# Kernel tuning notes

Measured on AMD Instinct MI355X. Metric: run time of the kernel, lower is better.

Reference implementation:

```python
import jax, jax.numpy as jnp
import numpy as np

WS = [2048, 4096, 8192]
RS = [1, 2, 4]
OFFSET = 0
NEG = -1e30


def _causal_attn(xseg, Wq, Wk, Wv, Wo):
    """xseg: (b, s, m, c). Returns (out (b,s,m,c), denom (b,s,m)) where denom is
    the softmax denominator sum_j exp(score_ij) per query (computed stably via lse)."""
    c = xseg.shape[-1]
    m = xseg.shape[-2]
    q = jnp.einsum('bsmc,cd->bsmd', xseg, Wq)
    k = jnp.einsum('bsmc,cd->bsmd', xseg, Wk)
    v = jnp.einsum('bsmc,cd->bsmd', xseg, Wv)
    scores = jnp.einsum('bsid,bsjd->bsij', q, k) / jnp.sqrt(jnp.asarray(c, xseg.dtype))
    causal = jnp.tril(jnp.ones((m, m), dtype=bool))
    scores = jnp.where(causal, scores, NEG)
    lse = jax.nn.logsumexp(scores, axis=-1)            # (b,s,m)
    p = jnp.exp(scores - lse[..., None])               # softmax
    o = jnp.einsum('bsij,bsjd->bsid', p, v)
    o = jnp.einsum('bsid,dc->bsic', o, Wo)
    return o, jnp.exp(lse)


def setup_inputs() -> dict:
    key = jax.random.key(0)
    kx, kq, kk, kv, ko = jax.random.split(key, 5)
    b, n, c = 4, 8192, 128
    scale = 1.0 / np.sqrt(c)  # keep activations O(1) so exp(lse) stays finite
    return {
        'x': jax.random.normal(kx, (b, n, c), dtype=jnp.float32),
        'Wq': jax.random.normal(kq, (c, c), dtype=jnp.float32) * scale,
        'Wk': jax.random.normal(kk, (c, c), dtype=jnp.float32) * scale,
        'Wv': jax.random.normal(kv, (c, c), dtype=jnp.float32) * scale,
        'Wo': jax.random.normal(ko, (c, c), dtype=jnp.float32) * scale,
    }


def reference(x, Wq, Wk, Wv, Wo):
    b, n, c = x.shape
    denom_sums = jnp.zeros((b, n), dtype=x.dtype)
    branches = []
    for w, r in zip(WS, RS):
        s = n // w
        # gather dilated tokens within each segment: (b, s, m, c)
        xr = x.reshape(b, s, w, c)[:, :, OFFSET::r, :]
        m = xr.shape[2]
        o, d = _causal_attn(xr, Wq, Wk, Wv, Wo)
        # global positions of the gathered tokens, flattened over (segment, within-seg)
        idx = (jnp.arange(s)[:, None] * w + OFFSET + r * jnp.arange(m)[None, :]).reshape(-1)
        d_flat = d.reshape(b, s * m)
        o_flat = o.reshape(b, s * m, c)
        denom_sums = denom_sums.at[:, idx].add(d_flat)
        branches.append((idx, o_flat, d_flat))
    out = jnp.zeros_like(x)
    for idx, o_flat, d_flat in branches:
        alpha = d_flat / denom_sums[:, idx]             # (b, s*m)
        out = out.at[:, idx].add(o_flat * alpha[..., None])
    return out
```

## Files before the change

kernel.cpp:

```cpp
#include <hip/hip_runtime.h>
#include <hip/hip_bf16.h>

typedef __attribute__((ext_vector_type(8))) __bf16 bf16x8;
typedef __attribute__((ext_vector_type(4))) float f32x4;
typedef __attribute__((ext_vector_type(8))) unsigned short u16x8;

#define DEVI __device__ __forceinline__
#define MFMA(a,b,c) __builtin_amdgcn_mfma_f32_16x16x32_bf16((a),(b),(c),0,0,0)
#define EXP2F(x) __builtin_exp2f(x)
#define LOG2F(x) __builtin_log2f(x)

DEVI unsigned short f2bf(float f){ __bf16 h = (__bf16)f; return __builtin_bit_cast(unsigned short, h); }
DEVI float bf2f(unsigned short u){ unsigned int x = ((unsigned int)u) << 16; return __builtin_bit_cast(float, x); }
DEVI bf16x8 ld_bf8(const void* p){ u16x8 u = *(const u16x8*)p; return __builtin_bit_cast(bf16x8, u); }
DEVI f32x4 splat4(float x){ f32x4 v = {x,x,x,x}; return v; }
DEVI f32x4 vmax4(f32x4 a, f32x4 b){
  f32x4 r;
  #pragma unroll
  for (int i=0;i<4;++i) r[i]=fmaxf(a[i],b[i]);
  return r;
}
DEVI void gload_lds16(const void* g, void* l){
  void* g2 = const_cast<void*>(g);
  __builtin_amdgcn_global_load_lds((__attribute__((address_space(1))) void*)g2,
                                   (__attribute__((address_space(3))) void*)l, 16, 0, 0);
}
#if __has_builtin(__builtin_amdgcn_permlane16_swap) && __has_builtin(__builtin_amdgcn_permlane32_swap)
DEVI float wavemax_hi(float x){
  unsigned int xu = __builtin_bit_cast(unsigned int, x);
  auto r1 = __builtin_amdgcn_permlane16_swap(xu, xu, false, false);
  float m = fmaxf(__builtin_bit_cast(float, (unsigned int)r1[0]),
                  __builtin_bit_cast(float, (unsigned int)r1[1]));
  unsigned int mu = __builtin_bit_cast(unsigned int, m);
  auto r2 = __builtin_amdgcn_permlane32_swap(mu, mu, false, false);
  return fmaxf(__builtin_bit_cast(float, (unsigned int)r2[0]),
               __builtin_bit_cast(float, (unsigned int)r2[1]));
}
#else
DEVI float wavemax_hi(float x){
  x = fmaxf(x, __shfl_xor(x, 16, 64));
  x = fmaxf(x, __shfl_xor(x, 32, 64));
  return x;
}
#endif

__device__ const unsigned int SCHED[30] = {
  0x100C000Bu, 0x110C0C0Bu, 0x050C0005u, 0x1C0B0A0Fu, 0x1D0B150Fu,
  0x0E0B000Au, 0x0F0B0B0Au, 0x1B0A000Fu, 0x180A000Eu, 0x190A0A0Eu,
  0x1A0A140Eu, 0x170A120Du, 0x0C0A0009u, 0x0D0A0A09u, 0x040A0004u,
  0x1509000Du, 0x1609090Du, 0x1309080Cu, 0x1409110Cu, 0x0A090008u,
  0x0B090908u, 0x1208000Cu, 0x08080007u, 0x09080807u, 0x03080003u,
  0x06070006u, 0x07070706u, 0x02060002u, 0x01040001u, 0x00020000u
};
__device__ const int CB[16] = {0,1,2,3,4,5,6,8,10,12,14,16,18,21,24,27};

__global__ __launch_bounds__(256) void k_prep(const float* __restrict__ Wq, const float* __restrict__ Wk,
                                              const float* __restrict__ Wv, const float* __restrict__ Wo,
                                              unsigned short* __restrict__ wT){
  int i = blockIdx.x*256 + threadIdx.x;
  int mat = i >> 14, col = (i >> 7) & 127, k = i & 127;
  const float* W = (mat==0)?Wq:(mat==1)?Wk:(mat==2)?Wv:Wo;
  float v = W[k*128 + col];
  if (mat == 0) v *= 0.12754245006257017f;
  wT[i] = f2bf(v);
}

__global__ __launch_bounds__(512) void k_qkv(const float* __restrict__ x, const unsigned short* __restrict__ wT,
                                             unsigned short* __restrict__ Qo, unsigned short* __restrict__ Ko,
                                             unsigned short* __restrict__ VT0, unsigned short* __restrict__ VT1,
                                             unsigned short* __restrict__ VT2){
  __shared__ unsigned short Tl[128*130];
  const int tid=threadIdx.x, lane=tid&63, wid=tid>>6, ll=lane&15, hi=lane>>4;
  const int row0g = blockIdx.x*128;
  const long row0 = (long)row0g + wid*16;
  bf16x8 a[4];
  {
    const float* xr = x + (row0 + ll)*128 + hi*8;
    #pragma unroll
    for (int ks=0;ks<4;++ks){
      f32x4 f0 = *(const f32x4*)(const void*)(xr + ks*32);
      f32x4 f1 = *(const f32x4*)(const void*)(xr + ks*32 + 4);
      u16x8 u;
      #pragma unroll
      for (int j=0;j<4;++j){ u[j]=f2bf(f0[j]); u[j+4]=f2bf(f1[j]); }
      a[ks] = __builtin_bit_cast(bf16x8, u);
    }
  }
  #pragma unroll
  for (int m3=0;m3<3;++m3){
    const unsigned short* wp = wT + m3*16384 + ll*128 + hi*8;
    #pragma unroll
    for (int nt=0;nt<8;++nt){
      f32x4 acc=splat4(0.f);
      #pragma unroll
      for (int ks=0;ks<4;++ks){
        bf16x8 b = ld_bf8(wp + nt*2048 + ks*32);
        acc = MFMA(a[ks], b, acc);
      }
      if (m3 < 2){
        unsigned short* outp = (m3==0)?Qo:Ko;
        #pragma unroll
        for (int r=0;r<4;++r)
          outp[(row0 + hi*4 + r)*128 + nt*16 + ll] = f2bf(acc[r]);
      } else {
        #pragma unroll
        for (int r=0;r<4;++r)
          Tl[(wid*16 + hi*4 + r)*130 + nt*16 + ll] = f2bf(acc[r]);
      }
    }
  }
  __syncthreads();
  int tk = 2*lane;
  int pp0 = (tk>>5)*32 + ((tk>>4)&1)*4 + ((tk&15)>>2)*8 + (tk&3);
  #pragma unroll 4
  for (int p=0;p<16;++p){
    int d = wid*16 + p;
    unsigned int w0 = (unsigned int)Tl[(2*lane)*130 + d] | ((unsigned int)Tl[(2*lane+1)*130 + d] << 16);
    *(unsigned int*)(VT0 + (long)d*32768 + row0g + pp0) = w0;
    if (lane < 32){
      unsigned int w1 = (unsigned int)Tl[(4*lane)*130 + d] | ((unsigned int)Tl[(4*lane+2)*130 + d] << 16);
      *(unsigned int*)(VT1 + (long)d*16384 + (row0g>>1) + pp0) = w1;
    }
    if (lane < 16){
      unsigned int w2 = (unsigned int)Tl[(8*lane)*130 + d] | ((unsigned int)Tl[(8*lane+4)*130 + d] << 16);
      *(unsigned int*)(VT2 + (long)d*8192 + (row0g>>2) + pp0) = w2;
    }
  }
}

__global__ __launch_bounds__(256,3) void k_attn(
    const unsigned short* __restrict__ Qg, const unsigned short* __restrict__ Kg,
    const unsigned short* __restrict__ VT0, const unsigned short* __restrict__ VT1,
    const unsigned short* __restrict__ VT2,
    unsigned short* __restrict__ OP, float* __restrict__ LP){
  __shared__ unsigned char smem[49152];

  const int tid=threadIdx.x, lane=tid&63, wid=tid>>6, ll=lane&15, hi=lane>>4;

  int x = blockIdx.x & 7;
  int i = blockIdx.x >> 3;
  int sid, r;
  if (i < 60){
    r = i >> 2; int k = i & 3;
    if (k < 3){ sid = 3*x + k; }
    else { sid = 24 + (x >> 1); if (x & 1) r += 15; }
  } else {
    int t = i - 60; r = 15 + t/3; sid = 3*x + t%3;
  }
  unsigned int e = SCHED[r];
  int qb   = (int)(e & 255u);
  int t032 = (int)((e >> 8) & 255u) * 2;
  int n32  = (int)((e >> 16) & 255u) * 2;
  int slot = (int)(e >> 24);
  int br, bb, seg;
  if (sid < 16){ br=0; bb=sid>>2; seg=sid&3; }
  else if (sid < 24){ br=1; bb=(sid-16)>>1; seg=(sid-16)&1; }
  else { br=2; bb=sid-24; seg=0; }
  const int rstr = 1 << br;
  const long g0 = (long)bb*8192 + (long)seg*(2048 << br);
  const int P = sid*30 + slot;
  const unsigned short* VTb = (br==0)?VT0:(br==1)?VT1:VT2;
  const int NC = 32768 >> br;
  const int rb0 = (int)(g0 >> br);

  const int qrow_w = qb*128 + wid*32;

  bf16x8 aq[2][4];
  #pragma unroll
  for (int mt=0;mt<2;++mt){
    long gq = g0 + (long)rstr*(qrow_w + mt*16 + ll);
    const unsigned short* qp = Qg + gq*128 + hi*8;
    #pragma unroll
    for (int ks=0;ks<4;++ks) aq[mt][ks] = ld_bf8(qp + ks*32);
  }

  f32x4 o[2][8];
  #pragma unroll
  for (int mt=0;mt<2;++mt){
    #pragma unroll
    for (int dt=0;dt<8;++dt) o[mt][dt]=splat4(0.f);
  }
  float mrun[2], lrun[2];
  mrun[0]=mrun[1]=0.f; lrun[0]=lrun[1]=0.f;

  const int m7 = ll & 7;
  int koffs[4];
  #pragma unroll
  for (int ks=0;ks<4;++ks) koffs[ks] = ll*256 + (((ks*4 + hi) ^ m7) * 16);
  const int voffb = ll*64 + (((hi + (ll >> 1)) & 3) * 16);

  const long kadv = (long)rstr*32*128;
  const unsigned short* ksrc0 = Kg + (g0 + (long)rstr*((long)t032*32 + wid*8 + hi))*128 + ((ll ^ hi) * 8);
  const unsigned short* ksrc1 = Kg + (g0 + (long)rstr*((long)t032*32 + wid*8 + 4 + hi))*128 + ((ll ^ (4 + hi)) * 8);
  const int d0_ = tid >> 2,        s0_ = tid & 3,        ga_ = (s0_ - (d0_ >> 1)) & 3;
  const int d1_ = (256+tid) >> 2,  s1_ = tid & 3,        gb_ = (s1_ - (d1_ >> 1)) & 3;
  const unsigned short* vsrc0 = VTb + (long)d0_*NC + rb0 + t032*32 + ga_*8;
  const unsigned short* vsrc1 = VTb + (long)d1_*NC + rb0 + t032*32 + gb_*8;

#define STAGE(bslot)                                                                   \
  {                                                                                    \
    unsigned char* Kb = smem + (bslot)*8192;                                           \
    unsigned char* Vb = smem + 24576 + (bslot)*8192;                                   \
    gload_lds16((const void*)ksrc0, (void*)(Kb + wid*2048));                           \
    gload_lds16((const void*)ksrc1, (void*)(Kb + wid*2048 + 1024));                    \
    gload_lds16((const void*)vsrc0, (void*)(Vb + wid*1024));                           \
    gload_lds16((const void*)vsrc1, (void*)(Vb + 4096 + wid*1024));                    \
    ksrc0 += kadv; ksrc1 += kadv; vsrc0 += 32; vsrc1 += 32;                            \
  }

  STAGE(0);
  STAGE(1);

  for (int it=0; it<n32; ++it){
    const int kt = t032 + it;
    if (it + 1 < n32){
      asm volatile("s_waitcnt vmcnt(4) lgkmcnt(0)" ::: "memory");
    } else {
      asm volatile("s_waitcnt vmcnt(0) lgkmcnt(0)" ::: "memory");
    }
    __builtin_amdgcn_s_barrier();
    __builtin_amdgcn_sched_barrier(0);

    if (it + 2 < n32){
      STAGE((it + 2) % 3);
    }

    if (kt*32 <= qrow_w + 31){
      unsigned char* Kc = smem + (it % 3)*8192;
      unsigned char* Vc = smem + 24576 + (it % 3)*8192;
      f32x4 s[2][2];
      #pragma unroll
      for (int mt=0;mt<2;++mt){
        #pragma unroll
        for (int nt=0;nt<2;++nt) s[mt][nt]=splat4(0.f);
      }
      #pragma unroll
      for (int nt=0;nt<2;++nt){
        #pragma unroll
        for (int ks=0;ks<4;++ks){
          bf16x8 bk = ld_bf8(Kc + koffs[ks] + nt*4096);
          s[0][nt] = MFMA(bk, aq[0][ks], s[0][nt]);
          s[1][nt] = MFMA(bk, aq[1][ks], s[1][nt]);
        }
      }
      if (kt*32 + 31 > qrow_w){
        #pragma unroll
        for (int mt=0;mt<2;++mt){
          int qrow = qrow_w + mt*16 + ll;
          #pragma unroll
          for (int nt=0;nt<2;++nt){
            int kvcol = kt*32 + nt*16 + hi*4;
            #pragma unroll
            for (int rr=0;rr<4;++rr) if (kvcol + rr > qrow) s[mt][nt][rr] = -1e30f;
          }
        }
      }
      bf16x8 pa[2];
      #pragma unroll
      for (int mt=0;mt<2;++mt){
        f32x4 ps[2];
        #pragma unroll
        for (int nt=0;nt<2;++nt){
          #pragma unroll
          for (int rr=0;rr<4;++rr) ps[nt][rr] = EXP2F(s[mt][nt][rr] - mrun[mt]);
        }
        f32x4 t4 = vmax4(s[mt][0], s[mt][1]);
        float mloc = fmaxf(fmaxf(t4[0],t4[1]), fmaxf(t4[2],t4[3]));
        mloc = wavemax_hi(mloc);
        bool upd = __any(mloc > mrun[mt] + 8.0f);
        float mnew = upd ? fmaxf(mrun[mt], mloc) : mrun[mt];
        float psc  = upd ? EXP2F(mrun[mt] - mnew) : 1.0f;
        mrun[mt] = mnew;
        f32x4 tsum = ps[0] + ps[1];
        lrun[mt] = psc * (lrun[mt] + (tsum[0]+tsum[1]) + (tsum[2]+tsum[3]));
        if (upd){
          f32x4 scv;
          #pragma unroll
          for (int rr=0;rr<4;++rr) scv[rr] = __shfl(psc, hi*4 + rr, 64);
          #pragma unroll
          for (int dt=0;dt<8;++dt) o[mt][dt] = o[mt][dt]*scv;
        }
        u16x8 up;
        #pragma unroll
        for (int rr=0;rr<4;++rr){
          up[rr]   = f2bf(ps[0][rr] * psc);
          up[4+rr] = f2bf(ps[1][rr] * psc);
        }
        pa[mt] = __builtin_bit_cast(bf16x8, up);
      }
      #pragma unroll
      for (int dt=0;dt<8;++dt){
        bf16x8 bv = ld_bf8(Vc + voffb + dt*1024);
        o[0][dt] = MFMA(pa[0], bv, o[0][dt]);
        o[1][dt] = MFMA(pa[1], bv, o[1][dt]);
      }
    }
  }
#undef STAGE

  unsigned short* op = OP + (long)P*16384;
  float* lp = LP + (long)P*128;
  #pragma unroll
  for (int mt=0;mt<2;++mt){
    float l = lrun[mt];
    l += __shfl_xor(l, 16, 64);
    l += __shfl_xor(l, 32, 64);
    float invs = 1.f / l;
    f32x4 iv;
    #pragma unroll
    for (int rr=0;rr<4;++rr) iv[rr] = __shfl(invs, hi*4 + rr, 64);
    #pragma unroll
    for (int dt=0;dt<8;++dt){
      f32x4 res = o[mt][dt]*iv;
      #pragma unroll
      for (int rr=0;rr<4;++rr){
        int qloc = wid*32 + mt*16 + hi*4 + rr;
        op[qloc*128 + dt*16 + ll] = f2bf(res[rr]);
      }
    }
    float lse = mrun[mt] + LOG2F(l);
    if (lane < 16){
      lp[wid*32 + mt*16 + lane] = lse;
    }
  }
}

__global__ __launch_bounds__(256) void k_comb(
    const unsigned short* __restrict__ OP, const float* __restrict__ LP,
    const unsigned short* __restrict__ wT, float* __restrict__ out){
  __shared__ float Wl[9*32];
  __shared__ unsigned short Tl[32*136];
  const int tid = threadIdx.x;
  const long G0 = (long)blockIdx.x * 32;
  const int bb = (int)(G0 >> 13);
  const int P0 = (int)(G0 & 8191);

  int pb[3], bn[3], qlb[3];
  {
    int sid0 = bb*4 + (P0 >> 11); int qb0 = (P0 & 2047) >> 7;
    pb[0] = sid0*30 + CB[qb0]; bn[0] = (qb0<6)?1:(qb0<12)?2:3; qlb[0] = P0 & 127;
    int p1b = P0 >> 1; int sid1 = 16 + bb*2 + (p1b >> 11); int qb1 = (p1b & 2047) >> 7;
    pb[1] = sid1*30 + CB[qb1]; bn[1] = (qb1<6)?1:(qb1<12)?2:3; qlb[1] = p1b & 127;
    int p2b = P0 >> 2; int sid2 = 24 + bb; int qb2 = p2b >> 7;
    pb[2] = sid2*30 + CB[qb2]; bn[2] = (qb2<6)?1:(qb2<12)?2:3; qlb[2] = p2b & 127;
  }

  if (tid < 32){
    int i = tid;
    float Lx[9];
    #pragma unroll
    for (int b=0;b<3;++b){
      bool pv = (i & ((1<<b)-1)) == 0;
      int ql = qlb[b] + (i >> b);
      #pragma unroll
      for (int c=0;c<3;++c){
        bool v = pv && (c < bn[b]);
        Lx[b*3+c] = v ? LP[(pb[b]+c)*128 + ql] : -1e30f;
      }
    }
    float mx = -1e30f;
    #pragma unroll
    for (int s=0;s<9;++s) mx = fmaxf(mx, Lx[s]);
    float W[9]; float wsum = 0.f;
    #pragma unroll
    for (int b=0;b<3;++b){
      bool pv = (i & ((1<<b)-1)) == 0;
      #pragma unroll
      for (int c=0;c<3;++c){
        bool v = pv && (c < bn[b]);
        W[b*3+c] = v ? EXP2F(Lx[b*3+c] - mx) : 0.f;
        wsum += W[b*3+c];
      }
    }
    float inv = 1.f / wsum;
    #pragma unroll
    for (int s=0;s<9;++s) Wl[s*32 + i] = W[s] * inv;
  }
  __syncthreads();

  {
    const int ch = tid & 15;
    const int r0 = tid >> 4;
    #pragma unroll
    for (int p=0;p<2;++p){
      int row = p*16 + r0;
      float y[8];
      #pragma unroll
      for (int j=0;j<8;++j) y[j] = 0.f;
      #pragma unroll
      for (int b=0;b<3;++b){
        if ((row & ((1<<b)-1)) == 0){
          int opr = qlb[b] + (row >> b);
          for (int c=0;c<bn[b];++c){
            float wgt = Wl[(b*3+c)*32 + row];
            const unsigned short* pp = OP + (long)(pb[b]+c)*16384 + opr*128 + ch*8;
            u16x8 u = *(const u16x8*)(const void*)pp;
            #pragma unroll
            for (int j=0;j<8;++j) y[j] += wgt * bf2f(u[j]);
          }
        }
      }
      u16x8 o;
      #pragma unroll
      for (int j=0;j<8;++j) o[j] = f2bf(y[j]);
      *(u16x8*)(void*)(Tl + row*136 + ch*8) = o;
    }
  }
  __syncthreads();

  {
    const int wv = tid >> 6, lane = tid & 63, ll = lane & 15, hi = lane >> 4;
    bf16x8 a[2][4];
    #pragma unroll
    for (int mt=0;mt<2;++mt){
      #pragma unroll
      for (int ks=0;ks<4;++ks)
        a[mt][ks] = ld_bf8(Tl + (mt*16 + ll)*136 + ks*32 + hi*8);
    }
    const unsigned short* wp = wT + 3*16384 + ll*128 + hi*8;
    #pragma unroll
    for (int t=0;t<2;++t){
      int nt = wv*2 + t;
      f32x4 acc0=splat4(0.f), acc1=splat4(0.f);
      #pragma unroll
      for (int ks=0;ks<4;++ks){
        bf16x8 b = ld_bf8(wp + nt*2048 + ks*32);
        acc0 = MFMA(a[0][ks], b, acc0);
        acc1 = MFMA(a[1][ks], b, acc1);
      }
      #pragma unroll
      for (int rr=0;rr<4;++rr){
        out[(G0 + hi*4 + rr)*128 + nt*16 + ll]      = acc0[rr];
        out[(G0 + 16 + hi*4 + rr)*128 + nt*16 + ll] = acc1[rr];
      }
    }
  }
}

extern "C" void kernel_launch(void* const* d_in, const int* in_sizes, int n_in,
                              void* d_out, int out_size, void* d_ws, size_t ws_size,
                              hipStream_t stream){
  const float* x  = (const float*)d_in[0];
  const float* Wq = (const float*)d_in[1];
  const float* Wk = (const float*)d_in[2];
  const float* Wv = (const float*)d_in[3];
  const float* Wo = (const float*)d_in[4];
  char* ws = (char*)d_ws;
  unsigned short* wT  = (unsigned short*)(ws);
  unsigned short* Q   = (unsigned short*)(ws + 131072);
  unsigned short* K   = (unsigned short*)(ws + 8519680);
  unsigned short* VT0 = (unsigned short*)(ws + 16908288);
  unsigned short* VT1 = (unsigned short*)(ws + 25296896);
  unsigned short* VT2 = (unsigned short*)(ws + 29491200);
  unsigned short* OP  = (unsigned short*)(ws + 31588352);
  float* LP           = (float*)(ws + 59113472);
  k_prep<<<256, 256, 0, stream>>>(Wq, Wk, Wv, Wo, wT);
  k_qkv <<<256, 512, 0, stream>>>(x, wT, Q, K, VT0, VT1, VT2);
  k_attn<<<840, 256, 0, stream>>>(Q, K, VT0, VT1, VT2, OP, LP);
  k_comb<<<1024, 256, 0, stream>>>(OP, LP, wT, (float*)d_out);
}
```

Before: 107.9 us.

## Split attention block across 8 waves of 16 query rows each

The attention kernel now uses 512 threads per block, with each wave owning 16 query rows instead of 32. The K/V staging per thread is halved to one K and one V load, and the wait count is adjusted to match. The online softmax now rescales before the exponent and starts the running max at -1e30. This gives more waves for latency hiding and fewer registers per wave, at the cost of each K/V LDS fragment being reused across fewer MFMAs per wave and more waves reading the same LDS data.

New measurement: 106.0 us. About the same (-1.8%).

```diff
diff --git a/kernel.cpp b/kernel.cpp
--- a/kernel.cpp
+++ b/kernel.cpp
@@ -128,7 +128,7 @@
   }
 }
 
-__global__ __launch_bounds__(256,3) void k_attn(
+__global__ __launch_bounds__(512,4) void k_attn(
     const unsigned short* __restrict__ Qg, const unsigned short* __restrict__ Kg,
     const unsigned short* __restrict__ VT0, const unsigned short* __restrict__ VT1,
     const unsigned short* __restrict__ VT2,
@@ -163,25 +163,20 @@
   const int NC = 32768 >> br;
   const int rb0 = (int)(g0 >> br);
 
-  const int qrow_w = qb*128 + wid*32;
-
-  bf16x8 aq[2][4];
+  const int qrow_w = qb*128 + wid*16;
+
+  bf16x8 aq[4];
+  {
+    long gq = g0 + (long)rstr*(qrow_w + ll);
+    const unsigned short* qp = Qg + gq*128 + hi*8;
+    #pragma unroll
+    for (int ks=0;ks<4;++ks) aq[ks] = ld_bf8(qp + ks*32);
+  }
+
+  f32x4 o[8];
   #pragma unroll
-  for (int mt=0;mt<2;++mt){
-    long gq = g0 + (long)rstr*(qrow_w + mt*16 + ll);
-    const unsigned short* qp = Qg + gq*128 + hi*8;
-    #pragma unroll
-    for (int ks=0;ks<4;++ks) aq[mt][ks] = ld_bf8(qp + ks*32);
-  }
-
-  f32x4 o[2][8];
-  #pragma unroll
-  for (int mt=0;mt<2;++mt){
-    #pragma unroll
-    for (int dt=0;dt<8;++dt) o[mt][dt]=splat4(0.f);
-  }
-  float mrun[2], lrun[2];
-  mrun[0]=mrun[1]=0.f; lrun[0]=lrun[1]=0.f;
+  for (int dt=0;dt<8;++dt) o[dt]=splat4(0.f);
+  float mrun=-1e30f, lrun=0.f;
 
   const int m7 = ll & 7;
   int koffs[4];
@@ -190,22 +185,18 @@
   const int voffb = ll*64 + (((hi + (ll >> 1)) & 3) * 16);
 
   const long kadv = (long)rstr*32*128;
-  const unsigned short* ksrc0 = Kg + (g0 + (long)rstr*((long)t032*32 + wid*8 + hi))*128 + ((ll ^ hi) * 8);
-  const unsigned short* ksrc1 = Kg + (g0 + (long)rstr*((long)t032*32 + wid*8 + 4 + hi))*128 + ((ll ^ (4 + hi)) * 8);
-  const int d0_ = tid >> 2,        s0_ = tid & 3,        ga_ = (s0_ - (d0_ >> 1)) & 3;
-  const int d1_ = (256+tid) >> 2,  s1_ = tid & 3,        gb_ = (s1_ - (d1_ >> 1)) & 3;
-  const unsigned short* vsrc0 = VTb + (long)d0_*NC + rb0 + t032*32 + ga_*8;
-  const unsigned short* vsrc1 = VTb + (long)d1_*NC + rb0 + t032*32 + gb_*8;
+  const int krow_s = wid*4 + hi;
+  const unsigned short* ksrc = Kg + (g0 + (long)rstr*((long)t032*32 + krow_s))*128 + ((ll ^ (krow_s & 7)) * 8);
+  const int d0_ = tid >> 2, s0_ = tid & 3, ga_ = (s0_ - (d0_ >> 1)) & 3;
+  const unsigned short* vsrc = VTb + (long)d0_*NC + rb0 + t032*32 + ga_*8;
 
 #define STAGE(bslot)                                                                   \
   {                                                                                    \
     unsigned char* Kb = smem + (bslot)*8192;                                           \
     unsigned char* Vb = smem + 24576 + (bslot)*8192;                                   \
-    gload_lds16((const void*)ksrc0, (void*)(Kb + wid*2048));                           \
-    gload_lds16((const void*)ksrc1, (void*)(Kb + wid*2048 + 1024));                    \
-    gload_lds16((const void*)vsrc0, (void*)(Vb + wid*1024));                           \
-    gload_lds16((const void*)vsrc1, (void*)(Vb + 4096 + wid*1024));                    \
-    ksrc0 += kadv; ksrc1 += kadv; vsrc0 += 32; vsrc1 += 32;                            \
+    gload_lds16((const void*)ksrc, (void*)(Kb + wid*1024));                            \
+    gload_lds16((const void*)vsrc, (void*)(Vb + wid*1024));                            \
+    ksrc += kadv; vsrc += 32;                                                          \
   }
 
   STAGE(0);
@@ -214,7 +205,7 @@
   for (int it=0; it<n32; ++it){
     const int kt = t032 + it;
     if (it + 1 < n32){
-      asm volatile("s_waitcnt vmcnt(4) lgkmcnt(0)" ::: "memory");
+      asm volatile("s_waitcnt vmcnt(2) lgkmcnt(0)" ::: "memory");
     } else {
       asm volatile("s_waitcnt vmcnt(0) lgkmcnt(0)" ::: "memory");
     }
@@ -225,74 +216,67 @@
       STAGE((it + 2) % 3);
     }
 
-    if (kt*32 <= qrow_w + 31){
+    if (kt*32 <= qrow_w + 15){
       unsigned char* Kc = smem + (it % 3)*8192;
       unsigned char* Vc = smem + 24576 + (it % 3)*8192;
-      f32x4 s[2][2];
-      #pragma unroll
-      for (int mt=0;mt<2;++mt){
-        #pragma unroll
-        for (int nt=0;nt<2;++nt) s[mt][nt]=splat4(0.f);
-      }
+      f32x4 s[2];
+      s[0]=splat4(0.f); s[1]=splat4(0.f);
       #pragma unroll
       for (int nt=0;nt<2;++nt){
         #pragma unroll
         for (int ks=0;ks<4;++ks){
           bf16x8 bk = ld_bf8(Kc + koffs[ks] + nt*4096);
-          s[0][nt] = MFMA(bk, aq[0][ks], s[0][nt]);
-          s[1][nt] = MFMA(bk, aq[1][ks], s[1][nt]);
+          s[nt] = MFMA(bk, aq[ks], s[nt]);
         }
       }
       if (kt*32 + 31 > qrow_w){
-        #pragma unroll
-        for (int mt=0;mt<2;++mt){
-          int qrow = qrow_w + mt*16 + ll;
+        int qrow = qrow_w + ll;
+        #pragma unroll
+        for (int nt=0;nt<2;++nt){
+          int kvcol = kt*32 + nt*16 + hi*4;
           #pragma unroll
-          for (int nt=0;nt<2;++nt){
-            int kvcol = kt*32 + nt*16 + hi*4;
-            #pragma unroll
-            for (int rr=0;rr<4;++rr) if (kvcol + rr > qrow) s[mt][nt][rr] = -1e30f;
-          }
-        }
-      }
-      bf16x8 pa[2];
-      #pragma unroll
-      for (int mt=0;mt<2;++mt){
-        f32x4 ps[2];
+          for (int rr=0;rr<4;++rr) if (kvcol + rr > qrow) s[nt][rr] = -1e30f;
+        }
+      }
+      {
+        f32x4 t4 = vmax4(s[0], s[1]);
+        float mloc = fmaxf(fmaxf(t4[0],t4[1]), fmaxf(t4[2],t4[3]));
+        mloc = wavemax_hi(mloc);
+        bool upd = __any(mloc > mrun + 8.0f);
+        if (upd){
+          float mnew = fmaxf(mrun, mloc);
+          float sc = EXP2F(mrun - mnew);
+          mrun = mnew;
+          lrun *= sc;
+          f32x4 scv;
+          #pragma unroll
+          for (int rr=0;rr<4;++rr) scv[rr] = __shfl(sc, hi*4 + rr, 64);
+          #pragma unroll
+          for (int dt=0;dt<8;++dt) o[dt] = o[dt]*scv;
+        }
+        f32x4 tsum = splat4(0.f);
         #pragma unroll
         for (int nt=0;nt<2;++nt){
           #pragma unroll
-          for (int rr=0;rr<4;++rr) ps[nt][rr] = EXP2F(s[mt][nt][rr] - mrun[mt]);
-        }
-        f32x4 t4 = vmax4(s[mt][0], s[mt][1]);
-        float mloc = fmaxf(fmaxf(t4[0],t4[1]), fmaxf(t4[2],t4[3]));
-        mloc = wavemax_hi(mloc);
-        bool upd = __any(mloc > mrun[mt] + 8.0f);
-        float mnew = upd ? fmaxf(mrun[mt], mloc) : mrun[mt];
-        float psc  = upd ? EXP2F(mrun[mt] - mnew) : 1.0f;
-        mrun[mt] = mnew;
-        f32x4 tsum = ps[0] + ps[1];
-        lrun[mt] = psc * (lrun[mt] + (tsum[0]+tsum[1]) + (tsum[2]+tsum[3]));
-        if (upd){
-          f32x4 scv;
-          #pragma unroll
-          for (int rr=0;rr<4;++rr) scv[rr] = __shfl(psc, hi*4 + rr, 64);
-          #pragma unroll
-          for (int dt=0;dt<8;++dt) o[mt][dt] = o[mt][dt]*scv;
-        }
+          for (int rr=0;rr<4;++rr) s[nt][rr] = EXP2F(s[nt][rr] - mrun);
+          tsum += s[nt];
+        }
+        lrun += (tsum[0]+tsum[1]) + (tsum[2]+tsum[3]);
+      }
+      bf16x8 pa;
+      {
         u16x8 up;
         #pragma unroll
         for (int rr=0;rr<4;++rr){
-          up[rr]   = f2bf(ps[0][rr] * psc);
-          up[4+rr] = f2bf(ps[1][rr] * psc);
-        }
-        pa[mt] = __builtin_bit_cast(bf16x8, up);
+          up[rr]   = f2bf(s[0][rr]);
+          up[4+rr] = f2bf(s[1][rr]);
+        }
+        pa = __builtin_bit_cast(bf16x8, up);
       }
       #pragma unroll
       for (int dt=0;dt<8;++dt){
         bf16x8 bv = ld_bf8(Vc + voffb + dt*1024);
-        o[0][dt] = MFMA(pa[0], bv, o[0][dt]);
-        o[1][dt] = MFMA(pa[1], bv, o[1][dt]);
+        o[dt] = MFMA(pa, bv, o[dt]);
       }
     }
   }
@@ -300,9 +284,8 @@
 
   unsigned short* op = OP + (long)P*16384;
   float* lp = LP + (long)P*128;
-  #pragma unroll
-  for (int mt=0;mt<2;++mt){
-    float l = lrun[mt];
+  {
+    float l = lrun;
     l += __shfl_xor(l, 16, 64);
     l += __shfl_xor(l, 32, 64);
     float invs = 1.f / l;
@@ -311,16 +294,16 @@
     for (int rr=0;rr<4;++rr) iv[rr] = __shfl(invs, hi*4 + rr, 64);
     #pragma unroll
     for (int dt=0;dt<8;++dt){
-      f32x4 res = o[mt][dt]*iv;
+      f32x4 res = o[dt]*iv;
       #pragma unroll
       for (int rr=0;rr<4;++rr){
-        int qloc = wid*32 + mt*16 + hi*4 + rr;
+        int qloc = wid*16 + hi*4 + rr;
         op[qloc*128 + dt*16 + ll] = f2bf(res[rr]);
       }
     }
-    float lse = mrun[mt] + LOG2F(l);
+    float lse = mrun + LOG2F(l);
     if (lane < 16){
-      lp[wid*32 + mt*16 + lane] = lse;
+      lp[wid*16 + lane] = lse;
     }
   }
 }
@@ -456,6 +439,6 @@
   float* LP           = (float*)(ws + 59113472);
   k_prep<<<256, 256, 0, stream>>>(Wq, Wk, Wv, Wo, wT);
   k_qkv <<<256, 512, 0, stream>>>(x, wT, Q, K, VT0, VT1, VT2);
-  k_attn<<<840, 256, 0, stream>>>(Q, K, VT0, VT1, VT2, OP, LP);
+  k_attn<<<840, 512, 0, stream>>>(Q, K, VT0, VT1, VT2, OP, LP);
   k_comb<<<1024, 256, 0, stream>>>(OP, LP, wT, (float*)d_out);
 }
```
